# Kernel optimization log

Hardware: AMD Instinct MI355X
Metric: run time of the kernel (lower is better)

The kernel has to match this reference:

```python
import jax, jax.numpy as jnp
import numpy as np

NBIN = 25
DELTA = 2.0 / (NBIN - 1)
EPS_COS = 1e-8   # torch CosineSimilarity eps
EPS_P = 1e-16    # pNumerator init in original


def setup_inputs() -> dict:
    key = jax.random.key(0)
    k1, k2, k3 = jax.random.split(key, 3)
    B, N, M = 16, 50000, 128
    qX = jax.random.normal(k1, (B, M), dtype=jnp.float32)
    dXs = jax.random.normal(k2, (B, N, M), dtype=jnp.float32)
    labels = jax.random.randint(k3, (B, N), 0, 2, dtype=jnp.int32)
    return {"qX": qX, "dXs": dXs, "labels": labels}


def _qap(qX, dXs, labels_f):
    # cosine similarity, matching torch.nn.CosineSimilarity (norms clamped at eps)
    num = jnp.einsum("bm,bnm->bn", qX, dXs)                      # (B, N)
    qn = jnp.maximum(jnp.linalg.norm(qX, axis=-1), EPS_COS)      # (B,)
    dn = jnp.maximum(jnp.linalg.norm(dXs, axis=-1), EPS_COS)     # (B, N)
    sim = num / (qn[:, None] * dn)                               # (B, N)

    # soft assignment to NBIN triangular bins centered at 1 - m*DELTA
    centers = 1.0 - jnp.arange(NBIN, dtype=sim.dtype) * DELTA    # (NBIN,)
    sa = jnp.clip(1.0 - jnp.abs(sim[..., None] - centers) / DELTA, 0.0)  # (B, N, NBIN)

    # per-bin reductions (computed once), then cumulative sums replace the O(nBin^2) loop
    num_per_bin = jnp.einsum("bnk,bn->bk", sa, labels_f)         # dot(sa[:,n], labels)
    den_per_bin = jnp.sum(sa, axis=1)                            # dot(sa[:,n], ones)

    pDen = jnp.cumsum(num_per_bin, axis=1)                       # (B, NBIN)
    pNum = EPS_P + jnp.cumsum(den_per_bin, axis=1)
    precision = pDen / pNum
    recall = num_per_bin / jnp.sum(labels_f, axis=1, keepdims=True)

    ap = jnp.sum(precision * recall, axis=1)                     # (B,)
    return jnp.mean(ap)


def reference(qX, dXs, labels):
    labels_f = labels.astype(qX.dtype)
    return _qap(qX, dXs, labels_f)
```

## Files before the change

### kernel.cpp

```cpp
#include <hip/hip_runtime.h>
#include <math.h>

#define NBIN 25
#define T 256
#define PAD 27
#define CHUNKS 64


__global__ __launch_bounds__(256)
void qap_accum(const float* __restrict__ qX, const float* __restrict__ dXs,
               const int* __restrict__ labels, float* __restrict__ ws, int N) {
    __shared__ float q[128];
    __shared__ float accN[T * PAD];
    __shared__ float accD[T * PAD];
    __shared__ float part[4 * 64];

    const int tid   = threadIdx.x;
    const int b     = blockIdx.x / CHUNKS;
    const int chunk = blockIdx.x % CHUNKS;

    if (tid < 128) q[tid] = qX[b * 128 + tid];
    for (int i = tid; i < T * PAD; i += T) { accN[i] = 0.f; accD[i] = 0.f; }
    __syncthreads();

    float qs = 0.f;
    #pragma unroll 8
    for (int j = 0; j < 128; ++j) qs = fmaf(q[j], q[j], qs);
    const float qn = fmaxf(sqrtf(qs), 1e-8f);

    const int per = (N + CHUNKS - 1) / CHUNKS;
    const int n0 = chunk * per;
    const int n1 = (n0 + per < N) ? (n0 + per) : N;

    const float4* q4 = reinterpret_cast<const float4*>(q);
    const int base = tid * PAD;
    float labCnt = 0.f;

    for (int n = n0 + tid; n < n1; n += T) {
        const float4* row =
            reinterpret_cast<const float4*>(dXs + ((size_t)b * N + n) * 128);
        float dot = 0.f, nrm = 0.f;
        #pragma unroll
        for (int j = 0; j < 32; ++j) {
            float4 x  = row[j];
            float4 qv = q4[j];
            dot = fmaf(x.x, qv.x, dot); dot = fmaf(x.y, qv.y, dot);
            dot = fmaf(x.z, qv.z, dot); dot = fmaf(x.w, qv.w, dot);
            nrm = fmaf(x.x, x.x, nrm);  nrm = fmaf(x.y, x.y, nrm);
            nrm = fmaf(x.z, x.z, nrm);  nrm = fmaf(x.w, x.w, nrm);
        }
        const float dn  = fmaxf(sqrtf(nrm), 1e-8f);
        const float sim = dot / (qn * dn);
        float p = (1.0f - sim) * 12.0f;
        p = fminf(fmaxf(p, 0.0f), 24.0f);
        int m = (int)p;
        if (m > 24) m = 24;
        const float frac = p - (float)m;
        const float lab  = (float)labels[(size_t)b * N + n];
        labCnt += lab;
        const float w0 = 1.0f - frac;
        accD[base + m] += w0;
        accN[base + m] += lab * w0;
        if (m + 1 < NBIN) {
            accD[base + m + 1] += frac;
            accN[base + m + 1] += lab * frac;
        }
    }
    accD[base + 25] = labCnt;
    __syncthreads();

    const int c  = tid & 63;
    const int qd = tid >> 6;
    if (c < 51) {
        const int idx = (c < 25) ? c : ((c < 50) ? (c - 25) : 25);
        const float* arr = (c < 25) ? accN : accD;
        float s = 0.f;
        const int t0 = qd * 64;
        #pragma unroll 8
        for (int t = t0; t < t0 + 64; ++t) s += arr[t * PAD + idx];
        part[qd * 64 + c] = s;
    }
    __syncthreads();
    if (tid < 51) {
        const float s = part[tid] + part[64 + tid] + part[128 + tid] + part[192 + tid];
        atomicAdd(&ws[b * 64 + tid], s);
    }
}

__global__ void qap_final(const float* __restrict__ ws, float* __restrict__ out, int B) {
    const int lane = threadIdx.x;
    float ap = 0.f;
    if (lane < B) {
        const float* w = ws + lane * 64;
        const float labSum = w[50];
        float cn = 0.f, cd = 0.f;
        for (int k = 0; k < NBIN; ++k) {
            const float nk = w[k];
            const float dk = w[25 + k];
            cn += nk;
            cd += dk;
            const float prec = cn / (1e-16f + cd);
            const float rec  = nk / labSum;
            ap = fmaf(prec, rec, ap);
        }
    }
    for (int off = 32; off > 0; off >>= 1) ap += __shfl_down(ap, off);
    if (lane == 0) out[0] = ap / (float)B;
}

extern "C" void kernel_launch(void* const* d_in, const int* in_sizes, int n_in,
                              void* d_out, int out_size, void* d_ws, size_t ws_size,
                              hipStream_t stream) {
    const float* qX     = (const float*)d_in[0];
    const float* dXs    = (const float*)d_in[1];
    const int*   labels = (const int*)d_in[2];
    float* out = (float*)d_out;
    float* ws  = (float*)d_ws;

    const int M = in_sizes[1] / in_sizes[2];
    const int B = in_sizes[0] / M;
    const int N = in_sizes[2] / B;
    (void)M;

    hipMemsetAsync(ws, 0, (size_t)B * 64 * sizeof(float), stream);
    qap_accum<<<B * CHUNKS, T, 0, stream>>>(qX, dXs, labels, ws, N);
    qap_final<<<1, 64, 0, stream>>>(ws, out, B);
}
```

Baseline: 541.7 us.

## Split each row across 8 lanes for coalesced loads with shuffle reduction

Each row's dot product and norm are now computed by 8 cooperating lanes that each load 4 float4s, then combined with xor shuffles. Before, one thread walked a whole 512-byte row, so adjacent lanes touched addresses far apart. The goal is coalesced global loads and a smaller shared-memory histogram (32 columns instead of 256), which should also raise occupancy. The cost is that only one lane in 8 does the binning, so that part runs with 1/8 of the threads active, plus extra shuffle work.

```diff
diff --git a/kernel.cpp b/kernel.cpp
--- a/kernel.cpp
+++ b/kernel.cpp
@@ -5,84 +5,107 @@
 #define T 256
 #define PAD 27
 #define CHUNKS 64
+#define NCOL 32
 
 
 __global__ __launch_bounds__(256)
 void qap_accum(const float* __restrict__ qX, const float* __restrict__ dXs,
                const int* __restrict__ labels, float* __restrict__ ws, int N) {
-    __shared__ float q[128];
-    __shared__ float accN[T * PAD];
-    __shared__ float accD[T * PAD];
-    __shared__ float part[4 * 64];
+    __shared__ float accN[NCOL * PAD];
+    __shared__ float accD[NCOL * PAD];
 
-    const int tid   = threadIdx.x;
+    const int tid = threadIdx.x;
     const int b     = blockIdx.x / CHUNKS;
     const int chunk = blockIdx.x % CHUNKS;
+    const int g = tid >> 3;
+    const int k = tid & 7;
 
-    if (tid < 128) q[tid] = qX[b * 128 + tid];
-    for (int i = tid; i < T * PAD; i += T) { accN[i] = 0.f; accD[i] = 0.f; }
-    __syncthreads();
+    for (int i = tid; i < NCOL * PAD; i += T) { accN[i] = 0.f; accD[i] = 0.f; }
+
+    const float4* q4 = reinterpret_cast<const float4*>(qX + (size_t)b * 128);
+    const float4 q0 = q4[k], q1 = q4[k + 8], q2 = q4[k + 16], q3 = q4[k + 24];
 
     float qs = 0.f;
-    #pragma unroll 8
-    for (int j = 0; j < 128; ++j) qs = fmaf(q[j], q[j], qs);
+    qs = fmaf(q0.x, q0.x, qs); qs = fmaf(q0.y, q0.y, qs);
+    qs = fmaf(q0.z, q0.z, qs); qs = fmaf(q0.w, q0.w, qs);
+    qs = fmaf(q1.x, q1.x, qs); qs = fmaf(q1.y, q1.y, qs);
+    qs = fmaf(q1.z, q1.z, qs); qs = fmaf(q1.w, q1.w, qs);
+    qs = fmaf(q2.x, q2.x, qs); qs = fmaf(q2.y, q2.y, qs);
+    qs = fmaf(q2.z, q2.z, qs); qs = fmaf(q2.w, q2.w, qs);
+    qs = fmaf(q3.x, q3.x, qs); qs = fmaf(q3.y, q3.y, qs);
+    qs = fmaf(q3.z, q3.z, qs); qs = fmaf(q3.w, q3.w, qs);
+    qs += __shfl_xor(qs, 1);
+    qs += __shfl_xor(qs, 2);
+    qs += __shfl_xor(qs, 4);
     const float qn = fmaxf(sqrtf(qs), 1e-8f);
 
     const int per = (N + CHUNKS - 1) / CHUNKS;
     const int n0 = chunk * per;
     const int n1 = (n0 + per < N) ? (n0 + per) : N;
 
-    const float4* q4 = reinterpret_cast<const float4*>(q);
-    const int base = tid * PAD;
+    __syncthreads();
+
+    const int base = g * PAD;
     float labCnt = 0.f;
 
-    for (int n = n0 + tid; n < n1; n += T) {
-        const float4* row =
-            reinterpret_cast<const float4*>(dXs + ((size_t)b * N + n) * 128);
-        float dot = 0.f, nrm = 0.f;
-        #pragma unroll
-        for (int j = 0; j < 32; ++j) {
-            float4 x  = row[j];
-            float4 qv = q4[j];
-            dot = fmaf(x.x, qv.x, dot); dot = fmaf(x.y, qv.y, dot);
-            dot = fmaf(x.z, qv.z, dot); dot = fmaf(x.w, qv.w, dot);
-            nrm = fmaf(x.x, x.x, nrm);  nrm = fmaf(x.y, x.y, nrm);
-            nrm = fmaf(x.z, x.z, nrm);  nrm = fmaf(x.w, x.w, nrm);
-        }
-        const float dn  = fmaxf(sqrtf(nrm), 1e-8f);
-        const float sim = dot / (qn * dn);
-        float p = (1.0f - sim) * 12.0f;
-        p = fminf(fmaxf(p, 0.0f), 24.0f);
-        int m = (int)p;
-        if (m > 24) m = 24;
-        const float frac = p - (float)m;
-        const float lab  = (float)labels[(size_t)b * N + n];
-        labCnt += lab;
-        const float w0 = 1.0f - frac;
-        accD[base + m] += w0;
-        accN[base + m] += lab * w0;
-        if (m + 1 < NBIN) {
-            accD[base + m + 1] += frac;
-            accN[base + m + 1] += lab * frac;
+    for (int nb = n0; nb < n1; nb += NCOL) {
+        const int n = nb + g;
+        if (n < n1) {
+            const float4* r4 =
+                reinterpret_cast<const float4*>(dXs + ((size_t)b * N + n) * 128);
+            const float4 x0 = r4[k], x1 = r4[k + 8], x2 = r4[k + 16], x3 = r4[k + 24];
+
+            float dot = 0.f, nrm = 0.f;
+            dot = fmaf(x0.x, q0.x, dot); dot = fmaf(x0.y, q0.y, dot);
+            dot = fmaf(x0.z, q0.z, dot); dot = fmaf(x0.w, q0.w, dot);
+            dot = fmaf(x1.x, q1.x, dot); dot = fmaf(x1.y, q1.y, dot);
+            dot = fmaf(x1.z, q1.z, dot); dot = fmaf(x1.w, q1.w, dot);
+            dot = fmaf(x2.x, q2.x, dot); dot = fmaf(x2.y, q2.y, dot);
+            dot = fmaf(x2.z, q2.z, dot); dot = fmaf(x2.w, q2.w, dot);
+            dot = fmaf(x3.x, q3.x, dot); dot = fmaf(x3.y, q3.y, dot);
+            dot = fmaf(x3.z, q3.z, dot); dot = fmaf(x3.w, q3.w, dot);
+            nrm = fmaf(x0.x, x0.x, nrm); nrm = fmaf(x0.y, x0.y, nrm);
+            nrm = fmaf(x0.z, x0.z, nrm); nrm = fmaf(x0.w, x0.w, nrm);
+            nrm = fmaf(x1.x, x1.x, nrm); nrm = fmaf(x1.y, x1.y, nrm);
+            nrm = fmaf(x1.z, x1.z, nrm); nrm = fmaf(x1.w, x1.w, nrm);
+            nrm = fmaf(x2.x, x2.x, nrm); nrm = fmaf(x2.y, x2.y, nrm);
+            nrm = fmaf(x2.z, x2.z, nrm); nrm = fmaf(x2.w, x2.w, nrm);
+            nrm = fmaf(x3.x, x3.x, nrm); nrm = fmaf(x3.y, x3.y, nrm);
+            nrm = fmaf(x3.z, x3.z, nrm); nrm = fmaf(x3.w, x3.w, nrm);
+
+            dot += __shfl_xor(dot, 1); nrm += __shfl_xor(nrm, 1);
+            dot += __shfl_xor(dot, 2); nrm += __shfl_xor(nrm, 2);
+            dot += __shfl_xor(dot, 4); nrm += __shfl_xor(nrm, 4);
+
+            if (k == 0) {
+                const float dn  = fmaxf(sqrtf(nrm), 1e-8f);
+                const float sim = dot / (qn * dn);
+                float p = (1.0f - sim) * 12.0f;
+                p = fminf(fmaxf(p, 0.0f), 24.0f);
+                int m = (int)p;
+                if (m > 24) m = 24;
+                const float frac = p - (float)m;
+                const float lab  = (float)labels[(size_t)b * N + n];
+                labCnt += lab;
+                const float w0 = 1.0f - frac;
+                accD[base + m] += w0;
+                accN[base + m] += lab * w0;
+                if (m + 1 < NBIN) {
+                    accD[base + m + 1] += frac;
+                    accN[base + m + 1] += lab * frac;
+                }
+            }
         }
     }
-    accD[base + 25] = labCnt;
+    if (k == 0) accD[base + 25] = labCnt;
     __syncthreads();
 
-    const int c  = tid & 63;
-    const int qd = tid >> 6;
-    if (c < 51) {
-        const int idx = (c < 25) ? c : ((c < 50) ? (c - 25) : 25);
-        const float* arr = (c < 25) ? accN : accD;
+    if (tid < 51) {
+        const int idx = (tid < 25) ? tid : ((tid < 50) ? (tid - 25) : 25);
+        const float* arr = (tid < 25) ? accN : accD;
         float s = 0.f;
-        const int t0 = qd * 64;
-        #pragma unroll 8
-        for (int t = t0; t < t0 + 64; ++t) s += arr[t * PAD + idx];
-        part[qd * 64 + c] = s;
-    }
-    __syncthreads();
-    if (tid < 51) {
-        const float s = part[tid] + part[64 + tid] + part[128 + tid] + part[192 + tid];
+        #pragma unroll
+        for (int c = 0; c < NCOL; ++c) s += arr[c * PAD + idx];
         atomicAdd(&ws[b * 64 + tid], s);
     }
 }
```

Result: no change. 542.0 us (+0.1%).
